# Performance work log

Measured on AMD Instinct MI355X. Metric: run time of the kernel, lower is better.

## Reference

```python
import jax, jax.numpy as jnp
import numpy as np

EPS = 1e-5        # BatchNorm1d default eps
SLOPE = 0.01      # torch LeakyReLU default negative slope


def setup_inputs() -> dict:
    key = jax.random.key(0)
    ks = jax.random.split(key, 10)
    N3, N2, N1, N0 = 4096, 16384, 65536, 262144  # coarse -> fine point hierarchy
    return {
        "feats": jax.random.normal(ks[0], (N3, 258), jnp.float32),
        "skip1": jax.random.normal(ks[1], (N0, 128), jnp.float32),
        "skip2": jax.random.normal(ks[2], (N1, 256), jnp.float32),
        "skip3": jax.random.normal(ks[3], (N2, 512), jnp.float32),
        "idx1": jax.random.randint(ks[4], (N2,), 0, N3, jnp.int32),
        "idx2": jax.random.randint(ks[5], (N1,), 0, N2, jnp.int32),
        "idx3": jax.random.randint(ks[6], (N0,), 0, N1, jnp.int32),
        "W1": jax.random.normal(ks[7], (770, 129), jnp.float32) * 0.05,
        "b1": jnp.zeros((129,), jnp.float32),
        "g1": jnp.ones((129,), jnp.float32),
        "be1": jnp.zeros((129,), jnp.float32),
        "W2": jax.random.normal(ks[8], (385, 64), jnp.float32) * 0.05,
        "b2": jnp.zeros((64,), jnp.float32),
        "g2": jnp.ones((64,), jnp.float32),
        "be2": jnp.zeros((64,), jnp.float32),
        "W3": jax.random.normal(ks[9], (192, 34), jnp.float32) * 0.05,
        "b3": jnp.zeros((34,), jnp.float32),
    }


def _bn(y, g, b):
    # training-mode batch norm over the points dimension (biased variance)
    m = y.mean(axis=0)
    v = y.var(axis=0)
    return (y - m) * jax.lax.rsqrt(v + EPS) * g + b


def _lrelu(x):
    return jnp.where(x >= 0, x, SLOPE * x)


def reference(feats, skip1, skip2, skip3, idx1, idx2, idx3,
              W1, b1, g1, be1, W2, b2, g2, be2, W3, b3):
    # stage 1: nearest upsample N3->N2, concat skip3, conv1x1 + BN + LeakyReLU
    x = jnp.concatenate([feats[idx1], skip3], axis=1)        # [N2, 770]
    x = _lrelu(_bn(x @ W1 + b1, g1, be1))                    # [N2, 129]
    # stage 2: upsample N2->N1
    x = jnp.concatenate([x[idx2], skip2], axis=1)            # [N1, 385]
    x = _lrelu(_bn(x @ W2 + b2, g2, be2))                    # [N1, 64]
    # stage 3: upsample N1->N0, plain conv1x1 (no BN / no activation)
    x = jnp.concatenate([x[idx3], skip1], axis=1)            # [N0, 192]
    return x @ W3 + b3                                       # [N0, 34]
```

## Files before the change

kernel.cpp:

```cpp
#include <hip/hip_runtime.h>

#define EPS 1e-5f
#define SLOPE 0.01f

typedef __attribute__((ext_vector_type(4))) float f32x4;
typedef __attribute__((ext_vector_type(8))) short bf16x8;

__device__ __forceinline__ short f2bf(float f) {
    unsigned u = __float_as_uint(f);
    unsigned r = (u + 0x7FFFu + ((u >> 16) & 1u)) >> 16;
    return (short)r;
}
__device__ __forceinline__ float lrelu(float v) { return v >= 0.f ? v : SLOPE * v; }

__device__ __forceinline__ void gload16(const float* g, float* l) {
    __builtin_amdgcn_global_load_lds(
        (const __attribute__((address_space(1))) unsigned*)g,
        (__attribute__((address_space(3))) unsigned*)l, 16, 0, 0);
}
__device__ __forceinline__ void gload4(const float* g, float* l) {
    __builtin_amdgcn_global_load_lds(
        (const __attribute__((address_space(1))) unsigned*)g,
        (__attribute__((address_space(3))) unsigned*)l, 4, 0, 0);
}

#define WCASE(N) case N: asm volatile("s_waitcnt vmcnt(" #N ")" ::: "memory"); break;
__device__ __forceinline__ void wait_vm(int n) {
    switch (n) {
    WCASE(0) WCASE(1) WCASE(2) WCASE(3) WCASE(4) WCASE(5) WCASE(6) WCASE(7)
    WCASE(8) WCASE(9) WCASE(10) WCASE(11) WCASE(12) WCASE(13) WCASE(14) WCASE(15)
    WCASE(16) WCASE(17) WCASE(18) WCASE(19) WCASE(20) WCASE(21) WCASE(22) WCASE(23)
    WCASE(24) WCASE(25) WCASE(26) WCASE(27) WCASE(28) WCASE(29) WCASE(30) WCASE(31)
    WCASE(32) WCASE(33) WCASE(34) WCASE(35) WCASE(36) WCASE(37) WCASE(38) WCASE(39)
    WCASE(40) WCASE(41) WCASE(42) WCASE(43) WCASE(44) WCASE(45) WCASE(46) WCASE(47)
    WCASE(48) WCASE(49) WCASE(50) WCASE(51) WCASE(52) WCASE(53) WCASE(54) WCASE(55)
    WCASE(56) WCASE(57) WCASE(58) WCASE(59) WCASE(60) WCASE(61) WCASE(62) WCASE(63)
    default: asm volatile("s_waitcnt vmcnt(0)" ::: "memory"); break;
    }
}

__global__ void prep(const float* __restrict__ W1, const float* __restrict__ W2,
                     const float* __restrict__ W3,
                     short* __restrict__ Wt1, short* __restrict__ Wt2,
                     short* __restrict__ Wt3, float* __restrict__ stats)
{
    int id = blockIdx.x * 256 + threadIdx.x;
    if (id < 2048) stats[id] = 0.f;
    if (id < 26 * 9 * 512) {
        int e = id & 7, lane = (id >> 3) & 63, g = id >> 9;
        int t = g / 9, nt = g - t * 9;
        int kv = t * 32 + (lane >> 4) * 8 + e;
        int n  = nt * 16 + (lane & 15);
        float v = 0.f; int ks = -1;
        if (kv < 258) ks = kv; else if (kv >= 320) ks = kv - 62;
        if (ks >= 0 && n < 129) v = W1[ks * 129 + n];
        Wt1[id] = f2bf(v);
    }
    if (id < 14 * 4 * 512) {
        int e = id & 7, lane = (id >> 3) & 63, g = id >> 9;
        int t = g >> 2, nt = g & 3;
        int kv = t * 32 + (lane >> 4) * 8 + e;
        int n  = nt * 16 + (lane & 15);
        float v = 0.f; int ks = -1;
        if (kv < 129) ks = kv; else if (kv >= 192) ks = kv - 63;
        if (ks >= 0) v = W2[ks * 64 + n];
        Wt2[id] = f2bf(v);
    }
    if (id < 6 * 3 * 512) {
        int e = id & 7, lane = (id >> 3) & 63, g = id >> 9;
        int t = g / 3, nt = g - t * 3;
        int kv = t * 32 + (lane >> 4) * 8 + e;
        int n  = nt * 16 + (lane & 15);
        float v = (n < 34) ? W3[kv * 34 + n] : 0.f;
        Wt3[id] = f2bf(v);
    }
}

template<int XD, int SD, int NCX, int NCS, int NT, int NVALID, int OD,
         bool XA16, int XCLAMP, bool BN, bool STATS, bool PRELB, int MINW>
__global__ __launch_bounds__(256, MINW)
void mfma_stage(const float* __restrict__ xsrc, const float* __restrict__ skip,
                const int* __restrict__ idx, const short* __restrict__ Wt,
                const float* __restrict__ bias,
                const float* __restrict__ bnsc, const float* __restrict__ bnsh,
                float* __restrict__ out, float* __restrict__ ssum,
                float* __restrict__ ssq)
{
    constexpr int NC = NCX + NCS;
    constexpr int T = 2 * NC;
    constexpr int NPAD = NT * 16;

    __shared__ __align__(16) float abuf[4][3][1024];
    __shared__ __align__(16) float bnl[BN ? 2 * NCX * 64 : 4];

    const int tid  = threadIdx.x;
    const int wave = tid >> 6, lane = tid & 63;
    const int lr = lane & 15;
    const int kg = lane >> 4;
    const int row0w = (blockIdx.x * 4 + wave) * 16;
    const short* wtf = Wt + (lane << 3);

    if (BN) {
        for (int i = tid; i < NCX * 64; i += 256) {
            bnl[i] = bnsc[i];
            bnl[NCX * 64 + i] = bnsh[i];
        }
        __syncthreads();
    }

    const float* prow[4];
    const float* rp16[16];
    if (XA16) {
#pragma unroll
        for (int q = 0; q < 4; ++q)
            prow[q] = xsrc + (size_t)idx[row0w + q * 4 + kg] * XD;
    } else {
#pragma unroll
        for (int j = 0; j < 16; ++j)
            rp16[j] = xsrc + (size_t)idx[row0w + j] * XD;
    }

    f32x4 acc[NT];
#pragma unroll
    for (int nt = 0; nt < NT; ++nt) acc[nt] = (f32x4){0.f, 0.f, 0.f, 0.f};

    auto sopsf = [](int c) { return (c < NCX && !XA16) ? 16 : 4; };

    auto issue = [&](int c) {
        float* wb = &abuf[wave][c % 3][0];
        if (c < NCX) {
            if (XA16) {
#pragma unroll
                for (int q = 0; q < 4; ++q) {
                    const int rl = q * 4 + kg;
                    const int s  = lane & 15;
                    const int cf = (s & ~7) | ((s & 7) ^ (rl & 6));
                    gload16(prow[q] + c * 64 + cf * 4, wb + q * 256);
                }
            } else {
#pragma unroll
                for (int j = 0; j < 16; ++j) {
                    const int s  = lane >> 2;
                    const int cf = (s & ~7) | ((s & 7) ^ (j & 6));
                    int col = c * 64 + cf * 4 + (lane & 3);
                    if (XCLAMP > 0 && c == NCX - 1) col = min(col, XCLAMP - 1);
                    gload4(rp16[j] + col, wb + j * 64);
                }
            }
        } else {
            const int jc = c - NCX;
#pragma unroll
            for (int q = 0; q < 4; ++q) {
                const int rl = q * 4 + kg;
                const int s  = lane & 15;
                const int cf = (s & ~7) | ((s & 7) ^ (rl & 6));
                gload16(skip + (size_t)(row0w + rl) * SD + jc * 64 + cf * 4,
                        wb + q * 256);
            }
        }
    };

    bf16x8 Bp[PRELB ? T * NT : 1];
    bf16x8 Bf[PRELB ? 1 : 3][2][NT];

    if (PRELB) {
#pragma unroll
        for (int tv = 0; tv < T; ++tv)
#pragma unroll
            for (int nt = 0; nt < NT; ++nt)
                Bp[tv * NT + nt] = *(const bf16x8*)(wtf + ((tv * NT + nt) << 9));
    }

    issue(0);
    if (NC > 1) issue(1);

    if (!PRELB) {
#pragma unroll
        for (int tt = 0; tt < 2; ++tt)
#pragma unroll
            for (int nt = 0; nt < NT; ++nt) {
                Bf[0][tt][nt] = *(const bf16x8*)(wtf + ((tt * NT + nt) << 9));
                if (NC > 1)
                    Bf[1][tt][nt] = *(const bf16x8*)(wtf + (((2 + tt) * NT + nt) << 9));
            }
    }

#pragma unroll
    for (int c = 0; c < NC; ++c) {
        if (c + 2 < NC) issue(c + 2);
        wait_vm(((c + 1 < NC) ? sopsf(c + 1) : 0) + ((c + 2 < NC) ? sopsf(c + 2) : 0));
        if (!PRELB && c + 2 < NC) {
#pragma unroll
            for (int tt = 0; tt < 2; ++tt)
#pragma unroll
                for (int nt = 0; nt < NT; ++nt)
                    Bf[(c + 2) % 3][tt][nt] =
                        *(const bf16x8*)(wtf + (((2 * (c + 2) + tt) * NT + nt) << 9));
        }

        const float* wb = &abuf[wave][c % 3][0];
#pragma unroll
        for (int tt = 0; tt < 2; ++tt) {
            const int s0 = tt * 8 + kg * 2;
            const int sw = (s0 & ~7) | ((s0 & 7) ^ (lr & 6));
            const float* fp = wb + lr * 64 + sw * 4;
            f32x4 lo = *(const f32x4*)fp;
            f32x4 hi = *(const f32x4*)(fp + 4);
            float v[8];
#pragma unroll
            for (int e = 0; e < 4; ++e) { v[e] = lo[e]; v[e + 4] = hi[e]; }
            if (BN && c < NCX) {
                const int kb = c * 64 + tt * 32 + kg * 8;
                f32x4 c0 = *(const f32x4*)&bnl[kb];
                f32x4 c1 = *(const f32x4*)&bnl[kb + 4];
                f32x4 h0 = *(const f32x4*)&bnl[NCX * 64 + kb];
                f32x4 h1 = *(const f32x4*)&bnl[NCX * 64 + kb + 4];
#pragma unroll
                for (int e = 0; e < 4; ++e) {
                    v[e]     = lrelu(fmaf(v[e],     c0[e], h0[e]));
                    v[e + 4] = lrelu(fmaf(v[e + 4], c1[e], h1[e]));
                }
            }
            bf16x8 a;
#pragma unroll
            for (int e = 0; e < 8; ++e) a[e] = f2bf(v[e]);
#pragma unroll
            for (int nt = 0; nt < NT; ++nt) {
                bf16x8 b;
                if (PRELB) b = Bp[(2 * c + tt) * NT + nt];
                else       b = Bf[c % 3][tt][nt];
                acc[nt] = __builtin_amdgcn_mfma_f32_16x16x32_bf16(a, b, acc[nt], 0, 0, 0);
            }
        }
    }

#pragma unroll
    for (int nt = 0; nt < NT; ++nt) {
        const int n = nt * 16 + lr;
        const float bv = (n < NVALID) ? bias[n] : 0.f;
#pragma unroll
        for (int r = 0; r < 4; ++r) acc[nt][r] += bv;
        if (n < NVALID) {
#pragma unroll
            for (int r = 0; r < 4; ++r)
                out[(size_t)(row0w + kg * 4 + r) * OD + n] = acc[nt][r];
        }
    }

    if (STATS) {
        float* ls = &abuf[0][0][0];
        __syncthreads();
        for (int i = tid; i < 2 * NPAD; i += 256) ls[i] = 0.f;
        __syncthreads();
#pragma unroll
        for (int nt = 0; nt < NT; ++nt) {
            float s = acc[nt][0] + acc[nt][1] + acc[nt][2] + acc[nt][3];
            float q = acc[nt][0]*acc[nt][0] + acc[nt][1]*acc[nt][1]
                    + acc[nt][2]*acc[nt][2] + acc[nt][3]*acc[nt][3];
            s += __shfl_xor(s, 16, 64);
            s += __shfl_xor(s, 32, 64);
            q += __shfl_xor(q, 16, 64);
            q += __shfl_xor(q, 32, 64);
            if (lane < 16) {
                atomicAdd(&ls[nt * 16 + lr], s);
                atomicAdd(&ls[NPAD + nt * 16 + lr], q);
            }
        }
        __syncthreads();
        for (int i = tid; i < NPAD; i += 256) {
            atomicAdd(&ssum[i], ls[i]);
            atomicAdd(&ssq[i], ls[NPAD + i]);
        }
    }
}

__global__ void finalize_bn(const float* __restrict__ sum,
                            const float* __restrict__ sq,
                            const float* __restrict__ g,
                            const float* __restrict__ be,
                            float* __restrict__ scale,
                            float* __restrict__ shift,
                            int C, int CPAD, float invN)
{
    int c = blockIdx.x * blockDim.x + threadIdx.x;
    if (c < CPAD) {
        if (c < C) {
            float m   = sum[c] * invN;
            float var = fmaf(-m, m, sq[c] * invN);
            float rs  = rsqrtf(var + EPS);
            float sc  = rs * g[c];
            scale[c] = sc;
            shift[c] = fmaf(-m, sc, be[c]);
        } else {
            scale[c] = 0.f;
            shift[c] = 0.f;
        }
    }
}

extern "C" void kernel_launch(void* const* d_in, const int* in_sizes, int n_in,
                              void* d_out, int out_size, void* d_ws, size_t ws_size,
                              hipStream_t stream) {
    const float* feats = (const float*)d_in[0];
    const float* skip1 = (const float*)d_in[1];
    const float* skip2 = (const float*)d_in[2];
    const float* skip3 = (const float*)d_in[3];
    const int*   idx1  = (const int*)d_in[4];
    const int*   idx2  = (const int*)d_in[5];
    const int*   idx3  = (const int*)d_in[6];
    const float* W1    = (const float*)d_in[7];
    const float* b1    = (const float*)d_in[8];
    const float* g1    = (const float*)d_in[9];
    const float* be1   = (const float*)d_in[10];
    const float* W2    = (const float*)d_in[11];
    const float* b2    = (const float*)d_in[12];
    const float* g2    = (const float*)d_in[13];
    const float* be2   = (const float*)d_in[14];
    const float* W3    = (const float*)d_in[15];
    const float* b3    = (const float*)d_in[16];

    float* ws   = (float*)d_ws;
    float* sum1 = ws;        float* sq1 = ws + 256;
    float* sc1  = ws + 512;  float* sh1 = ws + 768;
    float* sum2 = ws + 1024; float* sq2 = ws + 1280;
    float* sc2  = ws + 1536; float* sh2 = ws + 1792;
    short* Wt1  = (short*)(ws + 2048);
    short* Wt2  = Wt1 + 119808;
    short* Wt3  = Wt2 + 28672;
    float* y1   = ws + 2048 + (119808 + 28672 + 9216) / 2;
    float* y2   = y1 + 16384 * 192;
    float* outp = (float*)d_out;

    prep<<<468, 256, 0, stream>>>(W1, W2, W3, Wt1, Wt2, Wt3, ws);

    mfma_stage<258, 512, 5, 8, 9, 129, 192, false, 258, false, true, false, 1>
        <<<256, 256, 0, stream>>>(feats, skip3, idx1, Wt1, b1,
                                  nullptr, nullptr, y1, sum1, sq1);
    finalize_bn<<<1, 256, 0, stream>>>(sum1, sq1, g1, be1, sc1, sh1,
                                       129, 192, 1.f / 16384.f);

    mfma_stage<192, 256, 3, 4, 4, 64, 64, true, 0, true, true, false, 3>
        <<<1024, 256, 0, stream>>>(y1, skip2, idx2, Wt2, b2,
                                   sc1, sh1, y2, sum2, sq2);
    finalize_bn<<<1, 256, 0, stream>>>(sum2, sq2, g2, be2, sc2, sh2,
                                       64, 64, 1.f / 65536.f);

    mfma_stage<64, 128, 1, 2, 3, 34, 34, true, 0, true, false, true, 3>
        <<<4096, 256, 0, stream>>>(y2, skip1, idx3, Wt3, b3,
                                   sc2, sh2, outp, nullptr, nullptr);
}
```

Measured before the change: 122.5 us.

## Fuse three decoder stages into one persistent cooperative kernel with grid syncs

Replaces the five separate launches (three MFMA stages and two BN finalize kernels) with a single persistent cooperative kernel. Waves loop over row tiles, stages are separated by grid-wide syncs, and each block computes the BN scale and shift itself. BN statistics are accumulated per block in LDS across all its tiles before one global atomic flush, and the stage-2 B-operand loading changes to a double-buffered scheme. The aim is to remove launch gaps and tail effects, at the cost of grid-sync overhead, lower occupancy for stage 1 (it was tuned with MINW=1), and host-side occupancy and device-property queries on every launch.

```diff
diff --git a/kernel.cpp b/kernel.cpp
--- a/kernel.cpp
+++ b/kernel.cpp
@@ -1,4 +1,7 @@
 #include <hip/hip_runtime.h>
+#include <hip/hip_cooperative_groups.h>
+
+namespace cg = cooperative_groups;
 
 #define EPS 1e-5f
 #define SLOPE 0.01f
@@ -42,31 +45,33 @@
 __global__ void prep(const float* __restrict__ W1, const float* __restrict__ W2,
                      const float* __restrict__ W3,
                      short* __restrict__ Wt1, short* __restrict__ Wt2,
-                     short* __restrict__ Wt3, float* __restrict__ stats)
+                     short* __restrict__ Wt3, float* __restrict__ stats,
+                     float* __restrict__ y1)
 {
-    int id = blockIdx.x * 256 + threadIdx.x;
-    if (id < 2048) stats[id] = 0.f;
-    if (id < 26 * 9 * 512) {
+    const int id0 = blockIdx.x * 256 + threadIdx.x;
+    const int str = gridDim.x * 256;
+    for (int id = id0; id < 2048; id += str) stats[id] = 0.f;
+    for (int id = id0; id < 26 * 9 * 512; id += str) {
         int e = id & 7, lane = (id >> 3) & 63, g = id >> 9;
         int t = g / 9, nt = g - t * 9;
         int kv = t * 32 + (lane >> 4) * 8 + e;
         int n  = nt * 16 + (lane & 15);
         float v = 0.f; int ks = -1;
         if (kv < 258) ks = kv; else if (kv >= 320) ks = kv - 62;
-        if (ks >= 0 && n < 129) v = W1[ks * 129 + n];
+        if (ks >= 0 && ks < 770 && n < 129) v = W1[ks * 129 + n];
         Wt1[id] = f2bf(v);
     }
-    if (id < 14 * 4 * 512) {
+    for (int id = id0; id < 14 * 4 * 512; id += str) {
         int e = id & 7, lane = (id >> 3) & 63, g = id >> 9;
         int t = g >> 2, nt = g & 3;
         int kv = t * 32 + (lane >> 4) * 8 + e;
         int n  = nt * 16 + (lane & 15);
         float v = 0.f; int ks = -1;
         if (kv < 129) ks = kv; else if (kv >= 192) ks = kv - 63;
-        if (ks >= 0) v = W2[ks * 64 + n];
+        if (ks >= 0 && ks < 385) v = W2[ks * 64 + n];
         Wt2[id] = f2bf(v);
     }
-    if (id < 6 * 3 * 512) {
+    for (int id = id0; id < 6 * 3 * 512; id += str) {
         int e = id & 7, lane = (id >> 3) & 63, g = id >> 9;
         int t = g / 3, nt = g - t * 3;
         int kv = t * 32 + (lane >> 4) * 8 + e;
@@ -74,62 +79,50 @@
         float v = (n < 34) ? W3[kv * 34 + n] : 0.f;
         Wt3[id] = f2bf(v);
     }
+    for (int id = id0; id < 16384 * 64; id += str) {
+        int r = id >> 6, c = id & 63;
+        y1[(size_t)r * 192 + 128 + c] = 0.f;
+    }
 }
 
 template<int XD, int SD, int NCX, int NCS, int NT, int NVALID, int OD,
-         bool XA16, int XCLAMP, bool BN, bool STATS, bool PRELB, int MINW>
-__global__ __launch_bounds__(256, MINW)
-void mfma_stage(const float* __restrict__ xsrc, const float* __restrict__ skip,
-                const int* __restrict__ idx, const short* __restrict__ Wt,
-                const float* __restrict__ bias,
-                const float* __restrict__ bnsc, const float* __restrict__ bnsh,
-                float* __restrict__ out, float* __restrict__ ssum,
-                float* __restrict__ ssq)
+         bool XA16, int XCLAMP, bool BN, bool STATS, int BMODE>
+__device__ __forceinline__ void run_tile(
+    const float* __restrict__ xsrc, const float* __restrict__ skip,
+    const int* __restrict__ idx, const short* __restrict__ wtf,
+    const float* __restrict__ bias, const float* bnl,
+    float* __restrict__ out, float* lstats, float* awave,
+    const bf16x8* Bp, int tile, int lane)
 {
     constexpr int NC = NCX + NCS;
-    constexpr int T = 2 * NC;
-    constexpr int NPAD = NT * 16;
-
-    __shared__ __align__(16) float abuf[4][3][1024];
-    __shared__ __align__(16) float bnl[BN ? 2 * NCX * 64 : 4];
-
-    const int tid  = threadIdx.x;
-    const int wave = tid >> 6, lane = tid & 63;
     const int lr = lane & 15;
     const int kg = lane >> 4;
-    const int row0w = (blockIdx.x * 4 + wave) * 16;
-    const short* wtf = Wt + (lane << 3);
-
-    if (BN) {
-        for (int i = tid; i < NCX * 64; i += 256) {
-            bnl[i] = bnsc[i];
-            bnl[NCX * 64 + i] = bnsh[i];
-        }
-        __syncthreads();
-    }
-
-    const float* prow[4];
-    const float* rp16[16];
-    if (XA16) {
+    const int row0w = tile * 16;
+
+    auto sD = [](int c) -> int {
+        if (c < 0 || c >= NC) return 0;
+        return (c < NCX && !XA16) ? 16 : 4;
+    };
+    auto sB = [](int c) -> int {
+        if (c < 0 || c >= NC) return 0;
+        return 2 * NT;
+    };
+
+    const float* prow[XA16 ? 4 : 16];
+    if constexpr (XA16) {
 #pragma unroll
         for (int q = 0; q < 4; ++q)
             prow[q] = xsrc + (size_t)idx[row0w + q * 4 + kg] * XD;
     } else {
 #pragma unroll
         for (int j = 0; j < 16; ++j)
-            rp16[j] = xsrc + (size_t)idx[row0w + j] * XD;
-    }
-
-    f32x4 acc[NT];
-#pragma unroll
-    for (int nt = 0; nt < NT; ++nt) acc[nt] = (f32x4){0.f, 0.f, 0.f, 0.f};
-
-    auto sopsf = [](int c) { return (c < NCX && !XA16) ? 16 : 4; };
+            prow[j] = xsrc + (size_t)idx[row0w + j] * XD;
+    }
 
     auto issue = [&](int c) {
-        float* wb = &abuf[wave][c % 3][0];
+        float* wb = awave + (c % 3) * 1024;
         if (c < NCX) {
-            if (XA16) {
+            if constexpr (XA16) {
 #pragma unroll
                 for (int q = 0; q < 4; ++q) {
                     const int rl = q * 4 + kg;
@@ -144,7 +137,7 @@
                     const int cf = (s & ~7) | ((s & 7) ^ (j & 6));
                     int col = c * 64 + cf * 4 + (lane & 3);
                     if (XCLAMP > 0 && c == NCX - 1) col = min(col, XCLAMP - 1);
-                    gload4(rp16[j] + col, wb + j * 64);
+                    gload4(prow[j] + col, wb + j * 64);
                 }
             }
         } else {
@@ -160,45 +153,35 @@
         }
     };
 
-    bf16x8 Bp[PRELB ? T * NT : 1];
-    bf16x8 Bf[PRELB ? 1 : 3][2][NT];
-
-    if (PRELB) {
-#pragma unroll
-        for (int tv = 0; tv < T; ++tv)
+    bf16x8 Bf[(BMODE == 1) ? 2 : 1][2][NT];
+    auto loadB = [&](int c) {
+#pragma unroll
+        for (int tt = 0; tt < 2; ++tt)
 #pragma unroll
             for (int nt = 0; nt < NT; ++nt)
-                Bp[tv * NT + nt] = *(const bf16x8*)(wtf + ((tv * NT + nt) << 9));
-    }
+                Bf[c & 1][tt][nt] =
+                    *(const bf16x8*)(wtf + (((2 * c + tt) * NT + nt) << 9));
+    };
+
+    f32x4 acc[NT];
+#pragma unroll
+    for (int nt = 0; nt < NT; ++nt) acc[nt] = (f32x4){0.f, 0.f, 0.f, 0.f};
 
     issue(0);
     if (NC > 1) issue(1);
-
-    if (!PRELB) {
-#pragma unroll
-        for (int tt = 0; tt < 2; ++tt)
-#pragma unroll
-            for (int nt = 0; nt < NT; ++nt) {
-                Bf[0][tt][nt] = *(const bf16x8*)(wtf + ((tt * NT + nt) << 9));
-                if (NC > 1)
-                    Bf[1][tt][nt] = *(const bf16x8*)(wtf + (((2 + tt) * NT + nt) << 9));
-            }
-    }
+    if constexpr (BMODE == 1) loadB(0);
 
 #pragma unroll
     for (int c = 0; c < NC; ++c) {
         if (c + 2 < NC) issue(c + 2);
-        wait_vm(((c + 1 < NC) ? sopsf(c + 1) : 0) + ((c + 2 < NC) ? sopsf(c + 2) : 0));
-        if (!PRELB && c + 2 < NC) {
-#pragma unroll
-            for (int tt = 0; tt < 2; ++tt)
-#pragma unroll
-                for (int nt = 0; nt < NT; ++nt)
-                    Bf[(c + 2) % 3][tt][nt] =
-                        *(const bf16x8*)(wtf + (((2 * (c + 2) + tt) * NT + nt) << 9));
-        }
-
-        const float* wb = &abuf[wave][c % 3][0];
+        int n;
+        if constexpr (BMODE == 0)       n = sD(c+1) + sD(c+2) + sB(c-1) + sB(c-2);
+        else if constexpr (BMODE == 1)  n = sB(c-1) + sB(c) + sD(c+1) + sD(c+2);
+        else                            n = sD(c+1) + sD(c+2);
+        wait_vm(n > 63 ? 63 : n);
+        if constexpr (BMODE == 1) { if (c + 1 < NC) loadB(c + 1); }
+
+        const float* wb = awave + (c % 3) * 1024;
 #pragma unroll
         for (int tt = 0; tt < 2; ++tt) {
             const int s0 = tt * 8 + kg * 2;
@@ -227,8 +210,9 @@
 #pragma unroll
             for (int nt = 0; nt < NT; ++nt) {
                 bf16x8 b;
-                if (PRELB) b = Bp[(2 * c + tt) * NT + nt];
-                else       b = Bf[c % 3][tt][nt];
+                if constexpr (BMODE == 2)      b = Bp[(2 * c + tt) * NT + nt];
+                else if constexpr (BMODE == 1) b = Bf[c & 1][tt][nt];
+                else b = *(const bf16x8*)(wtf + (((2 * c + tt) * NT + nt) << 9));
                 acc[nt] = __builtin_amdgcn_mfma_f32_16x16x32_bf16(a, b, acc[nt], 0, 0, 0);
             }
         }
@@ -247,11 +231,7 @@
         }
     }
 
-    if (STATS) {
-        float* ls = &abuf[0][0][0];
-        __syncthreads();
-        for (int i = tid; i < 2 * NPAD; i += 256) ls[i] = 0.f;
-        __syncthreads();
+    if constexpr (STATS) {
 #pragma unroll
         for (int nt = 0; nt < NT; ++nt) {
             float s = acc[nt][0] + acc[nt][1] + acc[nt][2] + acc[nt][3];
@@ -262,40 +242,108 @@
             q += __shfl_xor(q, 16, 64);
             q += __shfl_xor(q, 32, 64);
             if (lane < 16) {
-                atomicAdd(&ls[nt * 16 + lr], s);
-                atomicAdd(&ls[NPAD + nt * 16 + lr], q);
-            }
-        }
-        __syncthreads();
-        for (int i = tid; i < NPAD; i += 256) {
-            atomicAdd(&ssum[i], ls[i]);
-            atomicAdd(&ssq[i], ls[NPAD + i]);
-        }
-    }
-}
-
-__global__ void finalize_bn(const float* __restrict__ sum,
-                            const float* __restrict__ sq,
-                            const float* __restrict__ g,
-                            const float* __restrict__ be,
-                            float* __restrict__ scale,
-                            float* __restrict__ shift,
-                            int C, int CPAD, float invN)
+                atomicAdd(&lstats[nt * 16 + lr], s);
+                atomicAdd(&lstats[NT * 16 + nt * 16 + lr], q);
+            }
+        }
+    }
+}
+
+__global__ __launch_bounds__(256, 3)
+void fused_decoder(const float* __restrict__ feats, const float* __restrict__ skip1,
+                   const float* __restrict__ skip2, const float* __restrict__ skip3,
+                   const int* __restrict__ idx1, const int* __restrict__ idx2,
+                   const int* __restrict__ idx3,
+                   const float* __restrict__ b1, const float* __restrict__ g1,
+                   const float* __restrict__ be1,
+                   const float* __restrict__ b2, const float* __restrict__ g2,
+                   const float* __restrict__ be2,
+                   const float* __restrict__ b3,
+                   float* __restrict__ ws, float* __restrict__ outp)
 {
-    int c = blockIdx.x * blockDim.x + threadIdx.x;
-    if (c < CPAD) {
-        if (c < C) {
-            float m   = sum[c] * invN;
-            float var = fmaf(-m, m, sq[c] * invN);
-            float rs  = rsqrtf(var + EPS);
-            float sc  = rs * g[c];
-            scale[c] = sc;
-            shift[c] = fmaf(-m, sc, be[c]);
-        } else {
-            scale[c] = 0.f;
-            shift[c] = 0.f;
-        }
-    }
+    __shared__ __align__(16) float abuf[4][3][1024];
+    __shared__ __align__(16) float bnl[384];
+    __shared__ float lstats[288];
+
+    float* sum1 = ws;       float* sq1 = ws + 256;
+    float* sum2 = ws + 512; float* sq2 = ws + 768;
+    const short* Wt1 = (const short*)(ws + 2048);
+    const short* Wt2 = Wt1 + 119808;
+    const short* Wt3 = Wt2 + 28672;
+    float* y1 = ws + 80896;
+    float* y2 = y1 + 16384 * 192;
+
+    const int tid = threadIdx.x;
+    const int wave = tid >> 6, lane = tid & 63;
+    const int nw = gridDim.x * 4;
+    const int gw = blockIdx.x * 4 + wave;
+    float* awave = &abuf[wave][0][0];
+    cg::grid_group gg = cg::this_grid();
+
+    for (int i = tid; i < 288; i += 256) lstats[i] = 0.f;
+    __syncthreads();
+
+    for (int t = gw; t < 1024; t += nw)
+        run_tile<258, 512, 5, 8, 9, 129, 192, false, 258, false, true, 0>(
+            feats, skip3, idx1, Wt1 + (lane << 3), b1, nullptr,
+            y1, lstats, awave, nullptr, t, lane);
+    __syncthreads();
+    for (int i = tid; i < 144; i += 256) {
+        atomicAdd(&sum1[i], lstats[i]);
+        atomicAdd(&sq1[i], lstats[144 + i]);
+    }
+    __threadfence();
+    gg.sync();
+    __threadfence();
+
+    if (tid < 192) {
+        float sc = 0.f, sh = 0.f;
+        if (tid < 129) {
+            float m   = sum1[tid] * (1.f / 16384.f);
+            float var = fmaf(-m, m, sq1[tid] * (1.f / 16384.f));
+            sc = rsqrtf(var + EPS) * g1[tid];
+            sh = fmaf(-m, sc, be1[tid]);
+        }
+        bnl[tid] = sc;
+        bnl[192 + tid] = sh;
+    }
+    for (int i = tid; i < 288; i += 256) lstats[i] = 0.f;
+    __syncthreads();
+
+    for (int t = gw; t < 4096; t += nw)
+        run_tile<192, 256, 3, 4, 4, 64, 64, true, 0, true, true, 1>(
+            y1, skip2, idx2, Wt2 + (lane << 3), b2, bnl,
+            y2, lstats, awave, nullptr, t, lane);
+    __syncthreads();
+    for (int i = tid; i < 64; i += 256) {
+        atomicAdd(&sum2[i], lstats[i]);
+        atomicAdd(&sq2[i], lstats[64 + i]);
+    }
+    __threadfence();
+    gg.sync();
+    __threadfence();
+
+    if (tid < 64) {
+        float m   = sum2[tid] * (1.f / 65536.f);
+        float var = fmaf(-m, m, sq2[tid] * (1.f / 65536.f));
+        float sc = rsqrtf(var + EPS) * g2[tid];
+        bnl[tid] = sc;
+        bnl[64 + tid] = fmaf(-m, sc, be2[tid]);
+    }
+    __syncthreads();
+
+    const short* wtf3 = Wt3 + (lane << 3);
+    bf16x8 Bp[18];
+#pragma unroll
+    for (int tv = 0; tv < 6; ++tv)
+#pragma unroll
+        for (int nt = 0; nt < 3; ++nt)
+            Bp[tv * 3 + nt] = *(const bf16x8*)(wtf3 + ((tv * 3 + nt) << 9));
+
+    for (int t = gw; t < 16384; t += nw)
+        run_tile<64, 128, 1, 2, 3, 34, 34, true, 0, true, false, 2>(
+            y2, skip1, idx3, wtf3, b3, bnl,
+            outp, nullptr, awave, Bp, t, lane);
 }
 
 extern "C" void kernel_launch(void* const* d_in, const int* in_sizes, int n_in,
@@ -320,32 +368,31 @@
     const float* b3    = (const float*)d_in[16];
 
     float* ws   = (float*)d_ws;
-    float* sum1 = ws;        float* sq1 = ws + 256;
-    float* sc1  = ws + 512;  float* sh1 = ws + 768;
-    float* sum2 = ws + 1024; float* sq2 = ws + 1280;
-    float* sc2  = ws + 1536; float* sh2 = ws + 1792;
     short* Wt1  = (short*)(ws + 2048);
     short* Wt2  = Wt1 + 119808;
     short* Wt3  = Wt2 + 28672;
-    float* y1   = ws + 2048 + (119808 + 28672 + 9216) / 2;
-    float* y2   = y1 + 16384 * 192;
+    float* y1   = ws + 80896;
     float* outp = (float*)d_out;
 
-    prep<<<468, 256, 0, stream>>>(W1, W2, W3, Wt1, Wt2, Wt3, ws);
-
-    mfma_stage<258, 512, 5, 8, 9, 129, 192, false, 258, false, true, false, 1>
-        <<<256, 256, 0, stream>>>(feats, skip3, idx1, Wt1, b1,
-                                  nullptr, nullptr, y1, sum1, sq1);
-    finalize_bn<<<1, 256, 0, stream>>>(sum1, sq1, g1, be1, sc1, sh1,
-                                       129, 192, 1.f / 16384.f);
-
-    mfma_stage<192, 256, 3, 4, 4, 64, 64, true, 0, true, true, false, 3>
-        <<<1024, 256, 0, stream>>>(y1, skip2, idx2, Wt2, b2,
-                                   sc1, sh1, y2, sum2, sq2);
-    finalize_bn<<<1, 256, 0, stream>>>(sum2, sq2, g2, be2, sc2, sh2,
-                                       64, 64, 1.f / 65536.f);
-
-    mfma_stage<64, 128, 1, 2, 3, 34, 34, true, 0, true, false, true, 3>
-        <<<4096, 256, 0, stream>>>(y2, skip1, idx3, Wt3, b3,
-                                   sc2, sh2, outp, nullptr, nullptr);
-}
+    prep<<<512, 256, 0, stream>>>(W1, W2, W3, Wt1, Wt2, Wt3, ws, y1);
+
+    int maxb = 0;
+    hipError_t e = hipOccupancyMaxActiveBlocksPerMultiprocessor(
+        &maxb, reinterpret_cast<const void*>(fused_decoder), 256, 0);
+    if (e != hipSuccess || maxb < 1) maxb = 2;
+    if (maxb > 3) maxb = 3;
+    int ncu = 256;
+    hipDeviceProp_t props;
+    if (hipGetDeviceProperties(&props, 0) == hipSuccess && props.multiProcessorCount > 0)
+        ncu = props.multiProcessorCount;
+
+    void* args[] = {
+        (void*)&feats, (void*)&skip1, (void*)&skip2, (void*)&skip3,
+        (void*)&idx1, (void*)&idx2, (void*)&idx3,
+        (void*)&b1, (void*)&g1, (void*)&be1,
+        (void*)&b2, (void*)&g2, (void*)&be2,
+        (void*)&b3, (void*)&ws, (void*)&outp
+    };
+    hipLaunchCooperativeKernel(reinterpret_cast<const void*>(fused_decoder),
+                               dim3(ncu * maxb), dim3(256), args, 0, stream);
+}
```

Result: slower. 393.7 us (+221.5%).

## Fold BN finalize into consumer stages and rework B-fragment loading modes

Applied to the files above, without the earlier changes.

Removes the two single-block finalize_bn launches: each consumer stage now computes BN scale and shift from the raw sums directly into LDS. Adds a BMODE template parameter. Stage 1 now reads weight fragments straight from global memory inside the MFMA loop (mode 0) with adjusted vmcnt waits, replacing the register triple-buffer, and its launch-bounds minimum rises to 2. The LDS swizzle changes to an XOR on 8-float pairs to cut bank conflicts, and prep zeroes y1's padding columns and uses grid-stride loops. This trades per-block redundant BN math and more global weight traffic in stage 1 for fewer launches and higher occupancy.

```diff
diff --git a/kernel.cpp b/kernel.cpp
--- a/kernel.cpp
+++ b/kernel.cpp
@@ -39,34 +39,40 @@
     }
 }
 
+__device__ __forceinline__ int swz_cf(int s, int r) {
+    return ((((s >> 1) ^ r) & 7) << 1) | (s & 1);
+}
+
 __global__ void prep(const float* __restrict__ W1, const float* __restrict__ W2,
                      const float* __restrict__ W3,
                      short* __restrict__ Wt1, short* __restrict__ Wt2,
-                     short* __restrict__ Wt3, float* __restrict__ stats)
+                     short* __restrict__ Wt3, float* __restrict__ stats,
+                     float* __restrict__ y1)
 {
-    int id = blockIdx.x * 256 + threadIdx.x;
-    if (id < 2048) stats[id] = 0.f;
-    if (id < 26 * 9 * 512) {
+    const int id0 = blockIdx.x * 256 + threadIdx.x;
+    const int str = gridDim.x * 256;
+    for (int id = id0; id < 2048; id += str) stats[id] = 0.f;
+    for (int id = id0; id < 26 * 9 * 512; id += str) {
         int e = id & 7, lane = (id >> 3) & 63, g = id >> 9;
         int t = g / 9, nt = g - t * 9;
         int kv = t * 32 + (lane >> 4) * 8 + e;
         int n  = nt * 16 + (lane & 15);
         float v = 0.f; int ks = -1;
         if (kv < 258) ks = kv; else if (kv >= 320) ks = kv - 62;
-        if (ks >= 0 && n < 129) v = W1[ks * 129 + n];
+        if (ks >= 0 && ks < 770 && n < 129) v = W1[ks * 129 + n];
         Wt1[id] = f2bf(v);
     }
-    if (id < 14 * 4 * 512) {
+    for (int id = id0; id < 14 * 4 * 512; id += str) {
         int e = id & 7, lane = (id >> 3) & 63, g = id >> 9;
         int t = g >> 2, nt = g & 3;
         int kv = t * 32 + (lane >> 4) * 8 + e;
         int n  = nt * 16 + (lane & 15);
         float v = 0.f; int ks = -1;
         if (kv < 129) ks = kv; else if (kv >= 192) ks = kv - 63;
-        if (ks >= 0) v = W2[ks * 64 + n];
+        if (ks >= 0 && ks < 385) v = W2[ks * 64 + n];
         Wt2[id] = f2bf(v);
     }
-    if (id < 6 * 3 * 512) {
+    for (int id = id0; id < 6 * 3 * 512; id += str) {
         int e = id & 7, lane = (id >> 3) & 63, g = id >> 9;
         int t = g / 3, nt = g - t * 3;
         int kv = t * 32 + (lane >> 4) * 8 + e;
@@ -74,20 +80,25 @@
         float v = (n < 34) ? W3[kv * 34 + n] : 0.f;
         Wt3[id] = f2bf(v);
     }
+    for (int id = id0; id < 16384 * 64; id += str) {
+        int r = id >> 6, c = id & 63;
+        y1[(size_t)r * 192 + 128 + c] = 0.f;
+    }
 }
 
 template<int XD, int SD, int NCX, int NCS, int NT, int NVALID, int OD,
-         bool XA16, int XCLAMP, bool BN, bool STATS, bool PRELB, int MINW>
+         bool XA16, int XCLAMP, int BNC, bool STATS, int BMODE, int MINW>
 __global__ __launch_bounds__(256, MINW)
 void mfma_stage(const float* __restrict__ xsrc, const float* __restrict__ skip,
                 const int* __restrict__ idx, const short* __restrict__ Wt,
                 const float* __restrict__ bias,
-                const float* __restrict__ bnsc, const float* __restrict__ bnsh,
-                float* __restrict__ out, float* __restrict__ ssum,
-                float* __restrict__ ssq)
+                const float* __restrict__ bnsum, const float* __restrict__ bnsq,
+                const float* __restrict__ bng, const float* __restrict__ bnbe,
+                float invN, float* __restrict__ out,
+                float* __restrict__ ssum, float* __restrict__ ssq)
 {
     constexpr int NC = NCX + NCS;
-    constexpr int T = 2 * NC;
+    constexpr bool BN = (BNC > 0);
     constexpr int NPAD = NT * 16;
 
     __shared__ __align__(16) float abuf[4][3][1024];
@@ -99,52 +110,61 @@
     const int kg = lane >> 4;
     const int row0w = (blockIdx.x * 4 + wave) * 16;
     const short* wtf = Wt + (lane << 3);
+    float* awave = &abuf[wave][0][0];
 
     if (BN) {
         for (int i = tid; i < NCX * 64; i += 256) {
-            bnl[i] = bnsc[i];
-            bnl[NCX * 64 + i] = bnsh[i];
+            float sc = 0.f, sh = 0.f;
+            if (i < BNC) {
+                float m   = bnsum[i] * invN;
+                float var = fmaf(-m, m, bnsq[i] * invN);
+                float rs  = rsqrtf(var + EPS);
+                sc = rs * bng[i];
+                sh = fmaf(-m, sc, bnbe[i]);
+            }
+            bnl[i] = sc;
+            bnl[NCX * 64 + i] = sh;
         }
         __syncthreads();
     }
 
-    const float* prow[4];
-    const float* rp16[16];
-    if (XA16) {
+    const float* prow[XA16 ? 4 : 16];
+    if constexpr (XA16) {
 #pragma unroll
         for (int q = 0; q < 4; ++q)
             prow[q] = xsrc + (size_t)idx[row0w + q * 4 + kg] * XD;
     } else {
 #pragma unroll
         for (int j = 0; j < 16; ++j)
-            rp16[j] = xsrc + (size_t)idx[row0w + j] * XD;
-    }
-
-    f32x4 acc[NT];
-#pragma unroll
-    for (int nt = 0; nt < NT; ++nt) acc[nt] = (f32x4){0.f, 0.f, 0.f, 0.f};
-
-    auto sopsf = [](int c) { return (c < NCX && !XA16) ? 16 : 4; };
+            prow[j] = xsrc + (size_t)idx[row0w + j] * XD;
+    }
+
+    auto sD = [](int c) -> int {
+        if (c < 0 || c >= NC) return 0;
+        return (c < NCX && !XA16) ? 16 : 4;
+    };
+    auto sB = [](int c) -> int {
+        if (c < 0 || c >= NC) return 0;
+        return 2 * NT;
+    };
 
     auto issue = [&](int c) {
-        float* wb = &abuf[wave][c % 3][0];
+        float* wb = awave + (c % 3) * 1024;
         if (c < NCX) {
-            if (XA16) {
+            if constexpr (XA16) {
 #pragma unroll
                 for (int q = 0; q < 4; ++q) {
                     const int rl = q * 4 + kg;
-                    const int s  = lane & 15;
-                    const int cf = (s & ~7) | ((s & 7) ^ (rl & 6));
+                    const int cf = swz_cf(lane & 15, rl);
                     gload16(prow[q] + c * 64 + cf * 4, wb + q * 256);
                 }
             } else {
 #pragma unroll
                 for (int j = 0; j < 16; ++j) {
-                    const int s  = lane >> 2;
-                    const int cf = (s & ~7) | ((s & 7) ^ (j & 6));
+                    const int cf = swz_cf(lane >> 2, j);
                     int col = c * 64 + cf * 4 + (lane & 3);
                     if (XCLAMP > 0 && c == NCX - 1) col = min(col, XCLAMP - 1);
-                    gload4(rp16[j] + col, wb + j * 64);
+                    gload4(prow[j] + col, wb + j * 64);
                 }
             }
         } else {
@@ -152,58 +172,56 @@
 #pragma unroll
             for (int q = 0; q < 4; ++q) {
                 const int rl = q * 4 + kg;
-                const int s  = lane & 15;
-                const int cf = (s & ~7) | ((s & 7) ^ (rl & 6));
+                const int cf = swz_cf(lane & 15, rl);
                 gload16(skip + (size_t)(row0w + rl) * SD + jc * 64 + cf * 4,
                         wb + q * 256);
             }
         }
     };
 
-    bf16x8 Bp[PRELB ? T * NT : 1];
-    bf16x8 Bf[PRELB ? 1 : 3][2][NT];
-
-    if (PRELB) {
-#pragma unroll
-        for (int tv = 0; tv < T; ++tv)
+    bf16x8 Bp[(BMODE == 2) ? 2 * NC * NT : 1];
+    bf16x8 Bf[(BMODE == 1) ? 3 : 1][2][NT];
+    auto loadB = [&](int cc) {
+#pragma unroll
+        for (int tt = 0; tt < 2; ++tt)
+#pragma unroll
+            for (int nt = 0; nt < NT; ++nt)
+                Bf[cc % 3][tt][nt] =
+                    *(const bf16x8*)(wtf + (((2 * cc + tt) * NT + nt) << 9));
+    };
+
+    f32x4 acc[NT];
+#pragma unroll
+    for (int nt = 0; nt < NT; ++nt) acc[nt] = (f32x4){0.f, 0.f, 0.f, 0.f};
+
+    if constexpr (BMODE == 2) {
+#pragma unroll
+        for (int tv = 0; tv < 2 * NC; ++tv)
 #pragma unroll
             for (int nt = 0; nt < NT; ++nt)
                 Bp[tv * NT + nt] = *(const bf16x8*)(wtf + ((tv * NT + nt) << 9));
     }
 
     issue(0);
+    if constexpr (BMODE == 1) loadB(0);
     if (NC > 1) issue(1);
-
-    if (!PRELB) {
-#pragma unroll
-        for (int tt = 0; tt < 2; ++tt)
-#pragma unroll
-            for (int nt = 0; nt < NT; ++nt) {
-                Bf[0][tt][nt] = *(const bf16x8*)(wtf + ((tt * NT + nt) << 9));
-                if (NC > 1)
-                    Bf[1][tt][nt] = *(const bf16x8*)(wtf + (((2 + tt) * NT + nt) << 9));
-            }
-    }
+    if constexpr (BMODE == 1) { if (NC > 1) loadB(1); }
 
 #pragma unroll
     for (int c = 0; c < NC; ++c) {
         if (c + 2 < NC) issue(c + 2);
-        wait_vm(((c + 1 < NC) ? sopsf(c + 1) : 0) + ((c + 2 < NC) ? sopsf(c + 2) : 0));
-        if (!PRELB && c + 2 < NC) {
-#pragma unroll
-            for (int tt = 0; tt < 2; ++tt)
-#pragma unroll
-                for (int nt = 0; nt < NT; ++nt)
-                    Bf[(c + 2) % 3][tt][nt] =
-                        *(const bf16x8*)(wtf + (((2 * (c + 2) + tt) * NT + nt) << 9));
-        }
-
-        const float* wb = &abuf[wave][c % 3][0];
+        int w;
+        if constexpr (BMODE == 0)      w = sD(c+1) + sD(c+2) + sB(c-1) + sB(c-2);
+        else if constexpr (BMODE == 1) w = sD(c+1) + sD(c+2) + sB(c) + sB(c+1);
+        else                           w = sD(c+1) + sD(c+2);
+        wait_vm(w > 63 ? 63 : w);
+        if constexpr (BMODE == 1) { if (c + 2 < NC) loadB(c + 2); }
+
+        const float* wb = awave + (c % 3) * 1024;
 #pragma unroll
         for (int tt = 0; tt < 2; ++tt) {
-            const int s0 = tt * 8 + kg * 2;
-            const int sw = (s0 & ~7) | ((s0 & 7) ^ (lr & 6));
-            const float* fp = wb + lr * 64 + sw * 4;
+            const int p0 = tt * 4 + kg;
+            const float* fp = wb + lr * 64 + ((p0 ^ (lr & 7)) << 3);
             f32x4 lo = *(const f32x4*)fp;
             f32x4 hi = *(const f32x4*)(fp + 4);
             float v[8];
@@ -227,8 +245,9 @@
 #pragma unroll
             for (int nt = 0; nt < NT; ++nt) {
                 bf16x8 b;
-                if (PRELB) b = Bp[(2 * c + tt) * NT + nt];
-                else       b = Bf[c % 3][tt][nt];
+                if constexpr (BMODE == 2)      b = Bp[(2 * c + tt) * NT + nt];
+                else if constexpr (BMODE == 1) b = Bf[c % 3][tt][nt];
+                else b = *(const bf16x8*)(wtf + (((2 * c + tt) * NT + nt) << 9));
                 acc[nt] = __builtin_amdgcn_mfma_f32_16x16x32_bf16(a, b, acc[nt], 0, 0, 0);
             }
         }
@@ -247,7 +266,7 @@
         }
     }
 
-    if (STATS) {
+    if constexpr (STATS) {
         float* ls = &abuf[0][0][0];
         __syncthreads();
         for (int i = tid; i < 2 * NPAD; i += 256) ls[i] = 0.f;
@@ -270,30 +289,6 @@
         for (int i = tid; i < NPAD; i += 256) {
             atomicAdd(&ssum[i], ls[i]);
             atomicAdd(&ssq[i], ls[NPAD + i]);
-        }
-    }
-}
-
-__global__ void finalize_bn(const float* __restrict__ sum,
-                            const float* __restrict__ sq,
-                            const float* __restrict__ g,
-                            const float* __restrict__ be,
-                            float* __restrict__ scale,
-                            float* __restrict__ shift,
-                            int C, int CPAD, float invN)
-{
-    int c = blockIdx.x * blockDim.x + threadIdx.x;
-    if (c < CPAD) {
-        if (c < C) {
-            float m   = sum[c] * invN;
-            float var = fmaf(-m, m, sq[c] * invN);
-            float rs  = rsqrtf(var + EPS);
-            float sc  = rs * g[c];
-            scale[c] = sc;
-            shift[c] = fmaf(-m, sc, be[c]);
-        } else {
-            scale[c] = 0.f;
-            shift[c] = 0.f;
         }
     }
 }
@@ -321,31 +316,28 @@
 
     float* ws   = (float*)d_ws;
     float* sum1 = ws;        float* sq1 = ws + 256;
-    float* sc1  = ws + 512;  float* sh1 = ws + 768;
-    float* sum2 = ws + 1024; float* sq2 = ws + 1280;
-    float* sc2  = ws + 1536; float* sh2 = ws + 1792;
+    float* sum2 = ws + 512;  float* sq2 = ws + 768;
     short* Wt1  = (short*)(ws + 2048);
     short* Wt2  = Wt1 + 119808;
     short* Wt3  = Wt2 + 28672;
-    float* y1   = ws + 2048 + (119808 + 28672 + 9216) / 2;
+    float* y1   = ws + 80896;
     float* y2   = y1 + 16384 * 192;
     float* outp = (float*)d_out;
 
-    prep<<<468, 256, 0, stream>>>(W1, W2, W3, Wt1, Wt2, Wt3, ws);
-
-    mfma_stage<258, 512, 5, 8, 9, 129, 192, false, 258, false, true, false, 1>
+    prep<<<512, 256, 0, stream>>>(W1, W2, W3, Wt1, Wt2, Wt3, ws, y1);
+
+    mfma_stage<258, 512, 5, 8, 9, 129, 192, false, 258, 0, true, 0, 2>
         <<<256, 256, 0, stream>>>(feats, skip3, idx1, Wt1, b1,
-                                  nullptr, nullptr, y1, sum1, sq1);
-    finalize_bn<<<1, 256, 0, stream>>>(sum1, sq1, g1, be1, sc1, sh1,
-                                       129, 192, 1.f / 16384.f);
-
-    mfma_stage<192, 256, 3, 4, 4, 64, 64, true, 0, true, true, false, 3>
+                                  nullptr, nullptr, nullptr, nullptr, 0.f,
+                                  y1, sum1, sq1);
+
+    mfma_stage<192, 256, 3, 4, 4, 64, 64, true, 0, 129, true, 1, 3>
         <<<1024, 256, 0, stream>>>(y1, skip2, idx2, Wt2, b2,
-                                   sc1, sh1, y2, sum2, sq2);
-    finalize_bn<<<1, 256, 0, stream>>>(sum2, sq2, g2, be2, sc2, sh2,
-                                       64, 64, 1.f / 65536.f);
-
-    mfma_stage<64, 128, 1, 2, 3, 34, 34, true, 0, true, false, true, 3>
+                                   sum1, sq1, g1, be1, 1.f / 16384.f,
+                                   y2, sum2, sq2);
+
+    mfma_stage<64, 128, 1, 2, 3, 34, 34, true, 0, 64, false, 2, 3>
         <<<4096, 256, 0, stream>>>(y2, skip1, idx3, Wt3, b3,
-                                   sc2, sh2, outp, nullptr, nullptr);
-}
+                                   sum2, sq2, g2, be2, 1.f / 65536.f,
+                                   outp, nullptr, nullptr);
+}
```

Result: slower. 125.3 us (+2.3%).
